# Optimization experiments

Hardware: AMD Instinct MI355X
Metric: run time of the kernel (lower is better)

Reference implementation:

```python
import jax, jax.numpy as jnp
import numpy as np

B, S, HID = 2, 2048, 4096
H, KH, D = 32, 8, 128
WINDOW = 1024
THETA = 1000000.0


def setup_inputs() -> dict:
    key = jax.random.key(0)
    ks = jax.random.split(key, 5)
    scale = 0.02
    hidden_states = jax.random.normal(ks[0], (B, S, HID), dtype=jnp.float32)
    wq = jax.random.normal(ks[1], (HID, H * D), dtype=jnp.float32) * scale
    wk = jax.random.normal(ks[2], (HID, KH * D), dtype=jnp.float32) * scale
    wv = jax.random.normal(ks[3], (HID, KH * D), dtype=jnp.float32) * scale
    wo = jax.random.normal(ks[4], (H * D, HID), dtype=jnp.float32) * scale
    position_ids = jnp.broadcast_to(jnp.arange(S, dtype=jnp.int64 if jax.config.jax_enable_x64 else jnp.int32), (B, S))
    return {"hidden_states": hidden_states, "position_ids": position_ids,
            "wq": wq, "wk": wk, "wv": wv, "wo": wo}


def _rope_sin_cos(position_ids):
    # inv_freq over even dims, emb = concat(freqs, freqs) -> [b, s, D]
    inv_freq = 1.0 / (THETA ** (jnp.arange(0, D, 2, dtype=jnp.float32) / D))
    angles = position_ids.astype(jnp.float32)[..., None] * inv_freq  # [b, s, D/2]
    emb = jnp.concatenate([angles, angles], axis=-1)  # [b, s, D]
    return jnp.sin(emb)[:, None, :, :], jnp.cos(emb)[:, None, :, :]  # [b,1,s,D]


def _rotate_half(x):
    x1, x2 = jnp.split(x, 2, axis=-1)
    return jnp.concatenate([-x2, x1], axis=-1)


def _apply_rope(x, sin, cos):
    return x * cos + _rotate_half(x) * sin


def reference(hidden_states, position_ids, wq, wk, wv, wo):
    b, s, _ = hidden_states.shape
    # projections -> [b, heads, s, d]
    q = (hidden_states @ wq).reshape(b, s, H, D).transpose(0, 2, 1, 3)
    k = (hidden_states @ wk).reshape(b, s, KH, D).transpose(0, 2, 1, 3)
    v = (hidden_states @ wv).reshape(b, s, KH, D).transpose(0, 2, 1, 3)
    sin, cos = _rope_sin_cos(position_ids)
    q = _apply_rope(q, sin, cos)
    k = _apply_rope(k, sin, cos)
    # repeat kv heads for GQA: [b, KH, s, d] -> [b, H, s, d]
    rep = H // KH
    k = jnp.repeat(k, rep, axis=1)
    v = jnp.repeat(v, rep, axis=1)
    # sliding-window causal mask
    i = jnp.arange(s)[:, None]
    j = jnp.arange(s)[None, :]
    mask = (j <= i) & (i - j < WINDOW)  # [s, s]
    scores = jnp.einsum("bhqd,bhkd->bhqk", q, k) / jnp.sqrt(jnp.asarray(D, q.dtype))
    neg = jnp.finfo(scores.dtype).min
    scores = jnp.where(mask[None, None, :, :], scores, neg)
    attn = jax.nn.softmax(scores, axis=-1)
    out = jnp.einsum("bhqk,bhkd->bhqd", attn, v)
    out = out.transpose(0, 2, 1, 3).reshape(b, s, H * D)
    return out @ wo
```

## Files before the change

kernel.cpp:

```cpp
#include <hip/hip_runtime.h>
#include <hip/hip_bf16.h>
#include <math.h>

typedef __attribute__((ext_vector_type(8))) __bf16 bf16x8;
typedef __attribute__((ext_vector_type(4))) float f32x4;

#define MFMA16(a, b, c) __builtin_amdgcn_mfma_f32_16x16x32_bf16((a), (b), (c), 0, 0, 0)

__device__ inline void gld_lds16(const __hip_bfloat16* g, __hip_bfloat16* l) {
    __builtin_amdgcn_global_load_lds(
        (const __attribute__((address_space(1))) void*)g,
        (__attribute__((address_space(3))) void*)l, 16, 0, 0);
}

__global__ void cast_bf16_kernel(const float* __restrict__ in, __hip_bfloat16* __restrict__ out) {
    int i = (blockIdx.x * blockDim.x + threadIdx.x) * 4;
    float4 v = *(const float4*)(in + i);
    out[i + 0] = __float2bfloat16(v.x);
    out[i + 1] = __float2bfloat16(v.y);
    out[i + 2] = __float2bfloat16(v.z);
    out[i + 3] = __float2bfloat16(v.w);
}

__global__ void transpose_cast_kernel(const float* __restrict__ w, __hip_bfloat16* __restrict__ wt,
                                      int K, int N) {
    __shared__ float tile[32][33];
    int n0 = blockIdx.x * 32, k0 = blockIdx.y * 32;
    int tx = threadIdx.x;
    int ty = threadIdx.y;
#pragma unroll
    for (int r = 0; r < 4; r++) {
        int k = k0 + ty + r * 8;
        tile[ty + r * 8][tx] = w[(size_t)k * N + n0 + tx];
    }
    __syncthreads();
#pragma unroll
    for (int r = 0; r < 4; r++) {
        int n = n0 + ty + r * 8;
        wt[(size_t)n * K + k0 + tx] = __float2bfloat16(tile[tx][ty + r * 8]);
    }
}

struct GemmAcc {
    f32x4 acc[4][4];
};

template <typename EPILOGUE>
__device__ __forceinline__ void gemm128_bk64(
    const __hip_bfloat16* __restrict__ A, const __hip_bfloat16* __restrict__ Bt,
    int m0, int n0, int K, __hip_bfloat16* As, __hip_bfloat16* Bs, EPILOGUE epi) {
    int tid = threadIdx.x;
    int wave = tid >> 6, lane = tid & 63;
    int l15 = lane & 15, quad = lane >> 4;

    int lr = lane >> 3;
    int c8 = (lane & 7) ^ lr;
    const __hip_bfloat16* aG = A + (size_t)(m0 + wave * 8 + lr) * K + c8 * 8;
    const __hip_bfloat16* bG = Bt + (size_t)(n0 + wave * 8 + lr) * K + c8 * 8;
    __hip_bfloat16* aL = As + wave * 512;
    __hip_bfloat16* bL = Bs + wave * 512;

    int wm = wave & 1, wn = wave >> 1;
    int e3 = l15 & 7;
    int s0 = (quad ^ e3) * 8;
    int s1 = ((4 + quad) ^ e3) * 8;
    const __hip_bfloat16* afr = As + (wm * 64 + l15) * 64;
    const __hip_bfloat16* bfr = Bs + (wn * 64 + l15) * 64;

    f32x4 acc[4][4];
#pragma unroll
    for (int mi = 0; mi < 4; mi++)
#pragma unroll
        for (int ni = 0; ni < 4; ni++) acc[mi][ni] = (f32x4){0.f, 0.f, 0.f, 0.f};

    for (int k0 = 0; k0 < K; k0 += 64) {
#pragma unroll
        for (int i = 0; i < 4; i++) {
            gld_lds16(aG + k0 + (size_t)(i * 32) * K, aL + i * 2048);
            gld_lds16(bG + k0 + (size_t)(i * 32) * K, bL + i * 2048);
        }
        __syncthreads();
        bf16x8 a0[4], b0[4], a1[4], b1[4];
#pragma unroll
        for (int mi = 0; mi < 4; mi++) {
            a0[mi] = *(const bf16x8*)(afr + mi * 1024 + s0);
            a1[mi] = *(const bf16x8*)(afr + mi * 1024 + s1);
        }
#pragma unroll
        for (int ni = 0; ni < 4; ni++) {
            b0[ni] = *(const bf16x8*)(bfr + ni * 1024 + s0);
            b1[ni] = *(const bf16x8*)(bfr + ni * 1024 + s1);
        }
#pragma unroll
        for (int mi = 0; mi < 4; mi++)
#pragma unroll
            for (int ni = 0; ni < 4; ni++) {
                acc[mi][ni] = MFMA16(a0[mi], b0[ni], acc[mi][ni]);
                acc[mi][ni] = MFMA16(a1[mi], b1[ni], acc[mi][ni]);
            }
        __syncthreads();
    }
    epi(acc, wm, wn, l15, quad);
}

__global__ __launch_bounds__(256) void gemm_qkv_kernel(
    const __hip_bfloat16* __restrict__ Xb,
    const __hip_bfloat16* __restrict__ Wt,
    __hip_bfloat16* __restrict__ Qraw,
    __hip_bfloat16* __restrict__ Kraw,
    __hip_bfloat16* __restrict__ Vtt) {
    __shared__ __hip_bfloat16 As[128 * 64];
    __shared__ __hip_bfloat16 Bs[128 * 64];
    int m0 = blockIdx.y * 128, n0 = blockIdx.x * 128;
    gemm128_bk64(Xb, Wt, m0, n0, 4096, As, Bs,
        [&](f32x4 (&acc)[4][4], int wm, int wn, int l15, int quad) {
#pragma unroll
            for (int mi = 0; mi < 4; mi++) {
#pragma unroll
                for (int ni = 0; ni < 4; ni++) {
                    int n = n0 + wn * 64 + ni * 16 + l15;
#pragma unroll
                    for (int r = 0; r < 4; r++) {
                        int m = m0 + wm * 64 + mi * 16 + quad * 4 + r;
                        int bb = m >> 11, s = m & 2047;
                        __hip_bfloat16 hv = __float2bfloat16(acc[mi][ni][r]);
                        if (n < 4096) {
                            int hh = n >> 7, d = n & 127;
                            Qraw[(((size_t)(bb * 32 + hh)) * 2048 + s) * 128 + d] = hv;
                        } else if (n < 5120) {
                            int n2 = n - 4096, hh = n2 >> 7, d = n2 & 127;
                            Kraw[(((size_t)(bb * 8 + hh)) * 2048 + s) * 128 + d] = hv;
                        } else {
                            int n2 = n - 5120, hh = n2 >> 7, d = n2 & 127;
                            Vtt[((((size_t)(bb * 8 + hh)) * 32 + (s >> 6)) * 128 + d) * 64 + (s & 63)] = hv;
                        }
                    }
                }
            }
        });
}

__global__ __launch_bounds__(256) void gemm_out_kernel(
    const __hip_bfloat16* __restrict__ A, const __hip_bfloat16* __restrict__ Bt,
    float* __restrict__ C) {
    __shared__ __hip_bfloat16 As[128 * 64];
    __shared__ __hip_bfloat16 Bs[128 * 64];
    int m0 = blockIdx.y * 128, n0 = blockIdx.x * 128;
    gemm128_bk64(A, Bt, m0, n0, 4096, As, Bs,
        [&](f32x4 (&acc)[4][4], int wm, int wn, int l15, int quad) {
            const int N = 4096;
#pragma unroll
            for (int mi = 0; mi < 4; mi++) {
#pragma unroll
                for (int ni = 0; ni < 4; ni++) {
                    int n = n0 + wn * 64 + ni * 16 + l15;
#pragma unroll
                    for (int r = 0; r < 4; r++) {
                        int m = m0 + wm * 64 + mi * 16 + quad * 4 + r;
                        C[(size_t)m * N + n] = acc[mi][ni][r];
                    }
                }
            }
        });
}

__global__ void rope_kernel(__hip_bfloat16* __restrict__ x, const int* __restrict__ pos_ids,
                            int nheads) {
    int idx = blockIdx.x * blockDim.x + threadIdx.x;
    int d = idx & 63;
    int s = (idx >> 6) & 2047;
    int bh = idx >> 17;
    int b = bh / nheads;
    float p = (float)pos_ids[b * 2048 + s];
    float inv = exp2f(-(float)d * 0.31143075889f);
    float ang = p * inv;
    float sn, cs;
    __sincosf(ang, &sn, &cs);
    size_t base = ((size_t)bh * 2048 + s) * 128;
    float x1 = __bfloat162float(x[base + d]);
    float x2 = __bfloat162float(x[base + d + 64]);
    x[base + d]      = __float2bfloat16(x1 * cs - x2 * sn);
    x[base + d + 64] = __float2bfloat16(x2 * cs + x1 * sn);
}

__global__ __launch_bounds__(256) void attn_kernel(
    const __hip_bfloat16* __restrict__ Qb, const __hip_bfloat16* __restrict__ Kb,
    const __hip_bfloat16* __restrict__ Vtt, __hip_bfloat16* __restrict__ AO) {
    const int S = 2048, D = 128;
    __shared__ __hip_bfloat16 Ks[64 * 128];
    __shared__ __hip_bfloat16 Vs[128 * 64];
    __shared__ __hip_bfloat16 Pl[4][16][72];

    int tid = threadIdx.x;
    int wave = tid >> 6, lane = tid & 63;
    int l15 = lane & 15, quad = lane >> 4;
    int base = blockIdx.x * 64;
    int i0 = base + wave * 16;
    int h = blockIdx.y, b = blockIdx.z;
    int kh = h >> 2;
    const __hip_bfloat16* Qh = Qb + (size_t)(b * 32 + h) * S * D;
    const __hip_bfloat16* Kh = Kb + (size_t)(b * 8 + kh) * S * D;
    const __hip_bfloat16* Vh = Vtt + (size_t)(b * 8 + kh) * S * D;

    bf16x8 qf[4];
    {
        const __hip_bfloat16* qrow = Qh + (size_t)(i0 + l15) * D + quad * 8;
#pragma unroll
        for (int kk = 0; kk < 4; kk++) qf[kk] = *(const bf16x8*)(qrow + kk * 32);
    }
    f32x4 o[8];
#pragma unroll
    for (int f = 0; f < 8; f++) o[f] = (f32x4){0.f, 0.f, 0.f, 0.f};
    float lrow[4] = {0.f, 0.f, 0.f, 0.f};

    int kst = (base > 1023) ? ((base - 1023) & ~63) : 0;
    const float c2 = 0.12751878882f;
    int e3 = l15 & 7;

    for (int key0 = kst; key0 <= base; key0 += 64) {
#pragma unroll
        for (int i = 0; i < 4; i++) {
            int rb = wave * 16 + i * 4;
            int row = rb + (lane >> 4);
            int c = (lane & 15) ^ (row & 7);
            gld_lds16(Kh + (size_t)(key0 + row) * 128 + c * 8, Ks + rb * 128);
        }
        const __hip_bfloat16* Vtile = Vh + (size_t)(key0 >> 6) * (128 * 64);
#pragma unroll
        for (int i = 0; i < 4; i++) {
            int db = wave * 32 + i * 8;
            int row = db + (lane >> 3);
            int c = (lane & 7) ^ (row & 7);
            gld_lds16(Vtile + (size_t)row * 64 + c * 8, Vs + db * 64);
        }
        __syncthreads();

        bool alive = (key0 <= i0 + 15) && (key0 + 63 >= i0 - 1023);
        if (alive) {
            f32x4 sc[4];
#pragma unroll
            for (int kb = 0; kb < 4; kb++) {
                sc[kb] = (f32x4){0.f, 0.f, 0.f, 0.f};
                const __hip_bfloat16* krow = Ks + (kb * 16 + l15) * 128;
#pragma unroll
                for (int kk = 0; kk < 4; kk++) {
                    int slot = ((kk << 2) | quad) ^ e3;
                    bf16x8 kf = *(const bf16x8*)(krow + slot * 8);
                    sc[kb] = MFMA16(qf[kk], kf, sc[kb]);
                }
            }
            bool interior = (key0 + 63 <= i0) && (key0 >= i0 - 1008);
            if (interior) {
#pragma unroll
                for (int kb = 0; kb < 4; kb++)
#pragma unroll
                    for (int r = 0; r < 4; r++) {
                        float p = __builtin_amdgcn_exp2f(sc[kb][r] * c2);
                        lrow[r] += p;
                        Pl[wave][quad * 4 + r][kb * 16 + l15] = __float2bfloat16(p);
                    }
            } else {
#pragma unroll
                for (int kb = 0; kb < 4; kb++)
#pragma unroll
                    for (int r = 0; r < 4; r++) {
                        int i = i0 + quad * 4 + r;
                        int j = key0 + kb * 16 + l15;
                        float v = (j <= i && i - j < 1024) ? sc[kb][r] * c2 : -1e30f;
                        float p = __builtin_amdgcn_exp2f(v);
                        lrow[r] += p;
                        Pl[wave][quad * 4 + r][kb * 16 + l15] = __float2bfloat16(p);
                    }
            }
            bf16x8 pf0 = *(const bf16x8*)(&Pl[wave][l15][quad * 8]);
            bf16x8 pf1 = *(const bf16x8*)(&Pl[wave][l15][32 + quad * 8]);
            int s0 = quad ^ e3, s1 = (4 + quad) ^ e3;
#pragma unroll
            for (int f = 0; f < 8; f++) {
                const __hip_bfloat16* vrow = Vs + (f * 16 + l15) * 64;
                bf16x8 v0 = *(const bf16x8*)(vrow + s0 * 8);
                bf16x8 v1 = *(const bf16x8*)(vrow + s1 * 8);
                o[f] = MFMA16(pf0, v0, o[f]);
                o[f] = MFMA16(pf1, v1, o[f]);
            }
        }
        __syncthreads();
    }

#pragma unroll
    for (int r = 0; r < 4; r++) {
#pragma unroll
        for (int msk = 1; msk < 16; msk <<= 1) lrow[r] += __shfl_xor(lrow[r], msk, 64);
    }
#pragma unroll
    for (int r = 0; r < 4; r++) {
        int srow = i0 + quad * 4 + r;
        float invl = 1.f / lrow[r];
        __hip_bfloat16* orow = AO + ((size_t)(b * 2048 + srow) * 4096) + h * 128;
#pragma unroll
        for (int f = 0; f < 8; f++) orow[f * 16 + l15] = __float2bfloat16(o[f][r] * invl);
    }
}

extern "C" void kernel_launch(void* const* d_in, const int* in_sizes, int n_in,
                              void* d_out, int out_size, void* d_ws, size_t ws_size,
                              hipStream_t stream) {
    (void)in_sizes; (void)n_in; (void)out_size;
    const float* hidden = (const float*)d_in[0];
    const int* pos = (const int*)d_in[1];
    const float* wq = (const float*)d_in[2];
    const float* wk = (const float*)d_in[3];
    const float* wv = (const float*)d_in[4];
    const float* wo = (const float*)d_in[5];
    float* out = (float*)d_out;

    const int M = 4096;
    char* ws = (char*)d_ws;
    size_t off = 0;
    auto alloc = [&](size_t bytes) { char* p = ws + off; off += bytes; return p; };
    __hip_bfloat16* Xb    = (__hip_bfloat16*)alloc((size_t)M * 4096 * 2);
    __hip_bfloat16* Wqkvt = (__hip_bfloat16*)alloc((size_t)6144 * 4096 * 2);
    __hip_bfloat16* Wot   = (__hip_bfloat16*)alloc((size_t)4096 * 4096 * 2);
    __hip_bfloat16* Qb    = (__hip_bfloat16*)alloc((size_t)M * 4096 * 2);
    __hip_bfloat16* Kb    = (__hip_bfloat16*)alloc((size_t)M * 1024 * 2);
    __hip_bfloat16* Vtt   = (__hip_bfloat16*)alloc((size_t)M * 1024 * 2);
    __hip_bfloat16* AO    = (__hip_bfloat16*)alloc((size_t)M * 4096 * 2);
    if (off > ws_size) return;

    cast_bf16_kernel<<<(M * 4096) / 1024, 256, 0, stream>>>(hidden, Xb);
    dim3 tb(32, 8);
    transpose_cast_kernel<<<dim3(128, 128), tb, 0, stream>>>(wq, Wqkvt, 4096, 4096);
    transpose_cast_kernel<<<dim3(32, 128),  tb, 0, stream>>>(wk, Wqkvt + (size_t)4096 * 4096, 4096, 1024);
    transpose_cast_kernel<<<dim3(32, 128),  tb, 0, stream>>>(wv, Wqkvt + (size_t)5120 * 4096, 4096, 1024);
    transpose_cast_kernel<<<dim3(128, 128), tb, 0, stream>>>(wo, Wot, 4096, 4096);

    gemm_qkv_kernel<<<dim3(48, 32), 256, 0, stream>>>(Xb, Wqkvt, Qb, Kb, Vtt);

    rope_kernel<<<(2 * 32 * 2048 * 64) / 256, 256, 0, stream>>>(Qb, pos, 32);
    rope_kernel<<<(2 * 8 * 2048 * 64) / 256, 256, 0, stream>>>(Kb, pos, 8);

    attn_kernel<<<dim3(32, 32, 2), 256, 0, stream>>>(Qb, Kb, Vtt, AO);

    gemm_out_kernel<<<dim3(32, 32), 256, 0, stream>>>(AO, Wot, out);
}
```

Before: 793.3 us.

## Rewrite projection GEMMs as 256x256 double-buffered 8-wave phased pipeline

Both projection GEMMs move from a 128x128 tile with 4 waves and a single LDS buffer to a 256x256 tile with 8 waves and double-buffered LDS. Each K step is split into four MFMA phases, with the next tile's global-to-LDS loads interleaved between them using raw barriers, explicit waitcnts and setprio. The aim is to hide global load latency behind MFMA work and to raise data reuse per loaded byte. The cost is larger LDS and register use per block, and grids of only 384 and 256 blocks, which may underfill the GPU.

```diff
diff --git a/kernel.cpp b/kernel.cpp
--- a/kernel.cpp
+++ b/kernel.cpp
@@ -12,6 +12,14 @@
         (const __attribute__((address_space(1))) void*)g,
         (__attribute__((address_space(3))) void*)l, 16, 0, 0);
 }
+
+#define RAW_BARRIER() __builtin_amdgcn_s_barrier()
+#define WAIT_LGKM0()                                          \
+    do {                                                      \
+        asm volatile("s_waitcnt lgkmcnt(0)" ::: "memory");    \
+        __builtin_amdgcn_sched_barrier(0);                    \
+    } while (0)
+#define WAIT_VM(N) asm volatile("s_waitcnt vmcnt(" #N ")" ::: "memory")
 
 __global__ void cast_bf16_kernel(const float* __restrict__ in, __hip_bfloat16* __restrict__ out) {
     int i = (blockIdx.x * blockDim.x + threadIdx.x) * 4;
@@ -41,87 +49,168 @@
     }
 }
 
-struct GemmAcc {
-    f32x4 acc[4][4];
-};
+constexpr int TILE = 256 * 64;
 
 template <typename EPILOGUE>
-__device__ __forceinline__ void gemm128_bk64(
+__device__ __forceinline__ void gemm256_8phase(
     const __hip_bfloat16* __restrict__ A, const __hip_bfloat16* __restrict__ Bt,
     int m0, int n0, int K, __hip_bfloat16* As, __hip_bfloat16* Bs, EPILOGUE epi) {
     int tid = threadIdx.x;
     int wave = tid >> 6, lane = tid & 63;
     int l15 = lane & 15, quad = lane >> 4;
+    int wr = wave >> 2, wc = wave & 3;
 
     int lr = lane >> 3;
     int c8 = (lane & 7) ^ lr;
     const __hip_bfloat16* aG = A + (size_t)(m0 + wave * 8 + lr) * K + c8 * 8;
     const __hip_bfloat16* bG = Bt + (size_t)(n0 + wave * 8 + lr) * K + c8 * 8;
-    __hip_bfloat16* aL = As + wave * 512;
-    __hip_bfloat16* bL = Bs + wave * 512;
-
-    int wm = wave & 1, wn = wave >> 1;
+    int stRow = wave * 8;
+
     int e3 = l15 & 7;
     int s0 = (quad ^ e3) * 8;
     int s1 = ((4 + quad) ^ e3) * 8;
-    const __hip_bfloat16* afr = As + (wm * 64 + l15) * 64;
-    const __hip_bfloat16* bfr = Bs + (wn * 64 + l15) * 64;
-
-    f32x4 acc[4][4];
-#pragma unroll
-    for (int mi = 0; mi < 4; mi++)
+
+    f32x4 acc[8][4];
+#pragma unroll
+    for (int mi = 0; mi < 8; mi++)
 #pragma unroll
         for (int ni = 0; ni < 4; ni++) acc[mi][ni] = (f32x4){0.f, 0.f, 0.f, 0.f};
 
-    for (int k0 = 0; k0 < K; k0 += 64) {
-#pragma unroll
-        for (int i = 0; i < 4; i++) {
-            gld_lds16(aG + k0 + (size_t)(i * 32) * K, aL + i * 2048);
-            gld_lds16(bG + k0 + (size_t)(i * 32) * K, bL + i * 2048);
-        }
-        __syncthreads();
-        bf16x8 a0[4], b0[4], a1[4], b1[4];
+    const int NT = K >> 6;
+
+    auto stA = [&](int buf, int kt, int i) {
+        gld_lds16(aG + (size_t)kt * 64 + (size_t)(i * 64) * K,
+                  As + buf * TILE + (stRow + i * 64) * 64);
+    };
+    auto stB = [&](int buf, int kt, int i) {
+        gld_lds16(bG + (size_t)kt * 64 + (size_t)(i * 64) * K,
+                  Bs + buf * TILE + (stRow + i * 64) * 64);
+    };
+
+#pragma unroll
+    for (int i = 0; i < 4; i++) stA(0, 0, i);
+#pragma unroll
+    for (int i = 0; i < 4; i++) stB(0, 0, i);
+    {
+        int k1 = (1 < NT) ? 1 : 0;
+#pragma unroll
+        for (int i = 0; i < 4; i++) stA(1, k1, i);
+    }
+    WAIT_VM(4);
+    RAW_BARRIER();
+
+    int cur = 0;
+    for (int t = 0; t < NT; ++t) {
+        int ktB = (t + 1 < NT) ? t + 1 : NT - 1;
+        int ktA = (t + 2 < NT) ? t + 2 : NT - 1;
+        const __hip_bfloat16* af = As + cur * TILE + (wr * 128 + l15) * 64;
+        const __hip_bfloat16* bf = Bs + cur * TILE + (wc * 64 + l15) * 64;
+        bf16x8 a0[4][2], a1[4][2], b0[2][2], b1[2][2];
+
 #pragma unroll
         for (int mi = 0; mi < 4; mi++) {
-            a0[mi] = *(const bf16x8*)(afr + mi * 1024 + s0);
-            a1[mi] = *(const bf16x8*)(afr + mi * 1024 + s1);
-        }
-#pragma unroll
-        for (int ni = 0; ni < 4; ni++) {
-            b0[ni] = *(const bf16x8*)(bfr + ni * 1024 + s0);
-            b1[ni] = *(const bf16x8*)(bfr + ni * 1024 + s1);
-        }
+            a0[mi][0] = *(const bf16x8*)(af + mi * 1024 + s0);
+            a0[mi][1] = *(const bf16x8*)(af + mi * 1024 + s1);
+        }
+#pragma unroll
+        for (int ni = 0; ni < 2; ni++) {
+            b0[ni][0] = *(const bf16x8*)(bf + ni * 1024 + s0);
+            b0[ni][1] = *(const bf16x8*)(bf + ni * 1024 + s1);
+        }
+        stB(cur ^ 1, ktB, 0);
+        stB(cur ^ 1, ktB, 1);
+        RAW_BARRIER();
+        WAIT_LGKM0();
+        __builtin_amdgcn_s_setprio(1);
 #pragma unroll
         for (int mi = 0; mi < 4; mi++)
 #pragma unroll
-            for (int ni = 0; ni < 4; ni++) {
-                acc[mi][ni] = MFMA16(a0[mi], b0[ni], acc[mi][ni]);
-                acc[mi][ni] = MFMA16(a1[mi], b1[ni], acc[mi][ni]);
-            }
-        __syncthreads();
-    }
-    epi(acc, wm, wn, l15, quad);
-}
-
-__global__ __launch_bounds__(256) void gemm_qkv_kernel(
+            for (int ni = 0; ni < 2; ni++) {
+                acc[mi][ni] = MFMA16(a0[mi][0], b0[ni][0], acc[mi][ni]);
+                acc[mi][ni] = MFMA16(a0[mi][1], b0[ni][1], acc[mi][ni]);
+            }
+        __builtin_amdgcn_s_setprio(0);
+        RAW_BARRIER();
+
+#pragma unroll
+        for (int mi = 0; mi < 4; mi++) {
+            a1[mi][0] = *(const bf16x8*)(af + (mi + 4) * 1024 + s0);
+            a1[mi][1] = *(const bf16x8*)(af + (mi + 4) * 1024 + s1);
+        }
+        stB(cur ^ 1, ktB, 2);
+        stB(cur ^ 1, ktB, 3);
+        RAW_BARRIER();
+        WAIT_LGKM0();
+        __builtin_amdgcn_s_setprio(1);
+#pragma unroll
+        for (int mi = 0; mi < 4; mi++)
+#pragma unroll
+            for (int ni = 0; ni < 2; ni++) {
+                acc[mi + 4][ni] = MFMA16(a1[mi][0], b0[ni][0], acc[mi + 4][ni]);
+                acc[mi + 4][ni] = MFMA16(a1[mi][1], b0[ni][1], acc[mi + 4][ni]);
+            }
+        __builtin_amdgcn_s_setprio(0);
+        RAW_BARRIER();
+
+#pragma unroll
+        for (int ni = 0; ni < 2; ni++) {
+            b1[ni][0] = *(const bf16x8*)(bf + (ni + 2) * 1024 + s0);
+            b1[ni][1] = *(const bf16x8*)(bf + (ni + 2) * 1024 + s1);
+        }
+        stA(cur, ktA, 0);
+        stA(cur, ktA, 1);
+        RAW_BARRIER();
+        WAIT_LGKM0();
+        __builtin_amdgcn_s_setprio(1);
+#pragma unroll
+        for (int mi = 0; mi < 4; mi++)
+#pragma unroll
+            for (int ni = 0; ni < 2; ni++) {
+                acc[mi][ni + 2] = MFMA16(a0[mi][0], b1[ni][0], acc[mi][ni + 2]);
+                acc[mi][ni + 2] = MFMA16(a0[mi][1], b1[ni][1], acc[mi][ni + 2]);
+            }
+        __builtin_amdgcn_s_setprio(0);
+        RAW_BARRIER();
+
+        stA(cur, ktA, 2);
+        stA(cur, ktA, 3);
+        RAW_BARRIER();
+        __builtin_amdgcn_s_setprio(1);
+#pragma unroll
+        for (int mi = 0; mi < 4; mi++)
+#pragma unroll
+            for (int ni = 0; ni < 2; ni++) {
+                acc[mi + 4][ni + 2] = MFMA16(a1[mi][0], b1[ni][0], acc[mi + 4][ni + 2]);
+                acc[mi + 4][ni + 2] = MFMA16(a1[mi][1], b1[ni][1], acc[mi + 4][ni + 2]);
+            }
+        __builtin_amdgcn_s_setprio(0);
+        WAIT_VM(4);
+        RAW_BARRIER();
+        cur ^= 1;
+    }
+    WAIT_VM(0);
+    epi(acc, wr, wc, l15, quad);
+}
+
+__global__ __launch_bounds__(512, 2) void gemm_qkv_kernel(
     const __hip_bfloat16* __restrict__ Xb,
     const __hip_bfloat16* __restrict__ Wt,
     __hip_bfloat16* __restrict__ Qraw,
     __hip_bfloat16* __restrict__ Kraw,
     __hip_bfloat16* __restrict__ Vtt) {
-    __shared__ __hip_bfloat16 As[128 * 64];
-    __shared__ __hip_bfloat16 Bs[128 * 64];
-    int m0 = blockIdx.y * 128, n0 = blockIdx.x * 128;
-    gemm128_bk64(Xb, Wt, m0, n0, 4096, As, Bs,
-        [&](f32x4 (&acc)[4][4], int wm, int wn, int l15, int quad) {
-#pragma unroll
-            for (int mi = 0; mi < 4; mi++) {
+    __shared__ __hip_bfloat16 As[2 * TILE];
+    __shared__ __hip_bfloat16 Bs[2 * TILE];
+    int m0 = blockIdx.y * 256, n0 = blockIdx.x * 256;
+    gemm256_8phase(Xb, Wt, m0, n0, 4096, As, Bs,
+        [&](f32x4 (&acc)[8][4], int wr, int wc, int l15, int quad) {
+#pragma unroll
+            for (int mi = 0; mi < 8; mi++) {
 #pragma unroll
                 for (int ni = 0; ni < 4; ni++) {
-                    int n = n0 + wn * 64 + ni * 16 + l15;
+                    int n = n0 + wc * 64 + ni * 16 + l15;
 #pragma unroll
                     for (int r = 0; r < 4; r++) {
-                        int m = m0 + wm * 64 + mi * 16 + quad * 4 + r;
+                        int m = m0 + wr * 128 + mi * 16 + quad * 4 + r;
                         int bb = m >> 11, s = m & 2047;
                         __hip_bfloat16 hv = __float2bfloat16(acc[mi][ni][r]);
                         if (n < 4096) {
@@ -140,23 +229,23 @@
         });
 }
 
-__global__ __launch_bounds__(256) void gemm_out_kernel(
+__global__ __launch_bounds__(512, 2) void gemm_out_kernel(
     const __hip_bfloat16* __restrict__ A, const __hip_bfloat16* __restrict__ Bt,
     float* __restrict__ C) {
-    __shared__ __hip_bfloat16 As[128 * 64];
-    __shared__ __hip_bfloat16 Bs[128 * 64];
-    int m0 = blockIdx.y * 128, n0 = blockIdx.x * 128;
-    gemm128_bk64(A, Bt, m0, n0, 4096, As, Bs,
-        [&](f32x4 (&acc)[4][4], int wm, int wn, int l15, int quad) {
+    __shared__ __hip_bfloat16 As[2 * TILE];
+    __shared__ __hip_bfloat16 Bs[2 * TILE];
+    int m0 = blockIdx.y * 256, n0 = blockIdx.x * 256;
+    gemm256_8phase(A, Bt, m0, n0, 4096, As, Bs,
+        [&](f32x4 (&acc)[8][4], int wr, int wc, int l15, int quad) {
             const int N = 4096;
 #pragma unroll
-            for (int mi = 0; mi < 4; mi++) {
+            for (int mi = 0; mi < 8; mi++) {
 #pragma unroll
                 for (int ni = 0; ni < 4; ni++) {
-                    int n = n0 + wn * 64 + ni * 16 + l15;
+                    int n = n0 + wc * 64 + ni * 16 + l15;
 #pragma unroll
                     for (int r = 0; r < 4; r++) {
-                        int m = m0 + wm * 64 + mi * 16 + quad * 4 + r;
+                        int m = m0 + wr * 128 + mi * 16 + quad * 4 + r;
                         C[(size_t)m * N + n] = acc[mi][ni][r];
                     }
                 }
@@ -334,12 +423,12 @@
     transpose_cast_kernel<<<dim3(32, 128),  tb, 0, stream>>>(wv, Wqkvt + (size_t)5120 * 4096, 4096, 1024);
     transpose_cast_kernel<<<dim3(128, 128), tb, 0, stream>>>(wo, Wot, 4096, 4096);
 
-    gemm_qkv_kernel<<<dim3(48, 32), 256, 0, stream>>>(Xb, Wqkvt, Qb, Kb, Vtt);
+    gemm_qkv_kernel<<<dim3(24, 16), 512, 0, stream>>>(Xb, Wqkvt, Qb, Kb, Vtt);
 
     rope_kernel<<<(2 * 32 * 2048 * 64) / 256, 256, 0, stream>>>(Qb, pos, 32);
     rope_kernel<<<(2 * 8 * 2048 * 64) / 256, 256, 0, stream>>>(Kb, pos, 8);
 
     attn_kernel<<<dim3(32, 32, 2), 256, 0, stream>>>(Qb, Kb, Vtt, AO);
 
-    gemm_out_kernel<<<dim3(32, 32), 256, 0, stream>>>(AO, Wot, out);
-}
+    gemm_out_kernel<<<dim3(16, 16), 512, 0, stream>>>(AO, Wot, out);
+}
```

Measured after the change: 841.6 us. +6.1%, slower.
